# Kernel tuning notes

Measured on AMD Instinct MI355X. Metric: run time of the kernel, lower is better.

Reference implementation:

```python
import jax, jax.numpy as jnp
import numpy as np

B, T, D, H = 8, 2048, 1024, 128


def setup_inputs() -> dict:
    key = jax.random.key(0)
    k1, k2, k3, k4 = jax.random.split(key, 4)
    x = jax.random.normal(k1, (B, T, D), dtype=jnp.float32)
    # nn.Linear(D, H, bias=False): y = x @ W.T with W [H, D]; we store W as [D, H]
    Wq = jax.random.normal(k2, (D, H), dtype=jnp.float32) * (1.0 / np.sqrt(D))
    Wk = jax.random.normal(k3, (D, H), dtype=jnp.float32) * (1.0 / np.sqrt(D))
    Wv = jax.random.normal(k4, (D, H), dtype=jnp.float32) * (1.0 / np.sqrt(D))
    return {"x": x, "Wq": Wq, "Wk": Wk, "Wv": Wv}


def reference(x, Wq, Wk, Wv):
    # q, k, v projections (bias-free)
    q = jnp.einsum("btd,dh->bth", x, Wq)
    k = jnp.einsum("btd,dh->bth", x, Wk)
    v = jnp.einsum("btd,dh->bth", x, Wv)
    scale = 1.0 / jnp.sqrt(jnp.asarray(q.shape[-1], dtype=q.dtype))
    # full T x T score matrix, as in the original module
    scores = jnp.einsum("bqh,bkh->bqk", q, k) * scale
    T_ = x.shape[1]
    causal = jnp.tril(jnp.ones((T_, T_), dtype=bool))
    scores = jnp.where(causal[None, :, :], scores, -jnp.inf)
    weights = jax.nn.softmax(scores, axis=-1)
    # dropout is identity in eval mode (deterministic reference)
    return jnp.einsum("bqk,bkh->bqh", weights, v)
```

## Files before the change

kernel.cpp:

```cpp
#include <hip/hip_runtime.h>

typedef float  f32x4  __attribute__((ext_vector_type(4)));
typedef __bf16 bf16x8 __attribute__((ext_vector_type(8)));
typedef unsigned short u16;
typedef unsigned int   u32;
typedef u32 u32x4 __attribute__((ext_vector_type(4)));
typedef u16 u16x4 __attribute__((ext_vector_type(4)));
typedef u16 u16x8 __attribute__((ext_vector_type(8)));
typedef float f32x4v __attribute__((ext_vector_type(4)));

#define B_ 8
#define T_ 2048
#define D_ 1024
#define H_ 128
#define M_ (B_ * T_)

__device__ __forceinline__ u16 f2b(float f) {
  u32 u = __builtin_bit_cast(u32, f);
  u32 r = u + 0x7fffu + ((u >> 16) & 1u);
  return (u16)(r >> 16);
}

__global__ __launch_bounds__(256) void wt_kernel(const float* __restrict__ Wq,
                                                 const float* __restrict__ Wk,
                                                 const float* __restrict__ Wv,
                                                 u16* __restrict__ ws) {
  __shared__ u16 Ld[128 * 136];
  const float* W = (blockIdx.y == 0) ? Wq : (blockIdx.y == 1) ? Wk : Wv;
  u16* Wt = ws + (size_t)blockIdx.y * (D_ * H_);
  const int d0 = blockIdx.x * 128;
  const int t = threadIdx.x;
  for (int i = 0; i < 16; ++i) {
    int idx = i * 256 + t;
    int d = idx >> 5, h4 = (idx & 31) * 4;
    f32x4v wv = *(const f32x4v*)(W + (size_t)(d0 + d) * H_ + h4);
    u16x4 bv;
    bv[0] = f2b(wv[0]); bv[1] = f2b(wv[1]); bv[2] = f2b(wv[2]); bv[3] = f2b(wv[3]);
    *(u16x4*)(&Ld[d * 136 + h4]) = bv;
  }
  __syncthreads();
  for (int i = 0; i < 8; ++i) {
    int idx = i * 256 + t;
    int h = idx >> 4, d8 = (idx & 15) * 8;
    u16x8 ov;
    for (int j = 0; j < 8; ++j) ov[j] = Ld[(d8 + j) * 136 + h];
    *(u16x8*)(Wt + (size_t)h * D_ + d0 + d8) = ov;
  }
}

__global__ __launch_bounds__(256, 4) void qkv_gemm(const float* __restrict__ x,
                                                   const u16* __restrict__ Wt_all,
                                                   u16* __restrict__ Qb,
                                                   u16* __restrict__ Kb,
                                                   u16* __restrict__ Vt) {
  __shared__ __attribute__((aligned(16))) u16 As[32 * 40];
  __shared__ __attribute__((aligned(16))) u16 Bs[384 * 40];
  const int m0 = blockIdx.x * 32;
  const int t = threadIdx.x;
  const int lane = t & 63;
  const int w = t >> 6;
  const int wn = w * 96;
  const int li = lane & 15, q4 = lane >> 4;

  f32x4 acc[2][6];
  for (int i = 0; i < 2; ++i)
    for (int j = 0; j < 6; ++j) acc[i][j] = (f32x4){0.f, 0.f, 0.f, 0.f};

  f32x4v areg;
  u32x4 breg[6];
  const int arow = t >> 3, ac4 = (t & 7) * 4;

  auto load_tiles = [&](int kt) {
    const int k0 = kt * 32;
    areg = *(const f32x4v*)(x + (size_t)(m0 + arow) * D_ + k0 + ac4);
    for (int i2 = 0; i2 < 6; ++i2) {
      int idx = i2 * 256 + t;
      int row = idx >> 2, c8 = (idx & 3) * 8;
      breg[i2] = *(const u32x4*)(Wt_all + (size_t)row * D_ + k0 + c8);
    }
  };

  load_tiles(0);
  for (int kt = 0; kt < 32; ++kt) {
    __syncthreads();
    {
      u16x4 bv;
      bv[0] = f2b(areg[0]); bv[1] = f2b(areg[1]);
      bv[2] = f2b(areg[2]); bv[3] = f2b(areg[3]);
      *(u16x4*)(&As[arow * 40 + ac4]) = bv;
    }
    for (int i2 = 0; i2 < 6; ++i2) {
      int idx = i2 * 256 + t;
      int row = idx >> 2, c8 = (idx & 3) * 8;
      *(u32x4*)(&Bs[row * 40 + c8]) = breg[i2];
    }
    __syncthreads();
    if (kt + 1 < 32) load_tiles(kt + 1);

    bf16x8 af[2];
    for (int i = 0; i < 2; ++i)
      af[i] = *(const bf16x8*)(&As[(i * 16 + li) * 40 + q4 * 8]);
    for (int j = 0; j < 6; ++j) {
      bf16x8 bfr = *(const bf16x8*)(&Bs[(wn + j * 16 + li) * 40 + q4 * 8]);
      for (int i = 0; i < 2; ++i)
        acc[i][j] = __builtin_amdgcn_mfma_f32_16x16x32_bf16(af[i], bfr, acc[i][j], 0, 0, 0);
    }
  }

  const float qs = 0.12751740696864213f;
  const int bb = m0 >> 11;
  const int tl0 = (m0 & (T_ - 1)) + q4 * 4;
  for (int j = 0; j < 6; ++j) {
    int n = wn + j * 16 + li;
    int p = n >> 7, col = n & 127;
    if (p == 2) {
      for (int i = 0; i < 2; ++i) {
        u16x4 pv;
        for (int r = 0; r < 4; ++r) pv[r] = f2b(acc[i][j][r]);
        *(u16x4*)(Vt + (size_t)bb * (H_ * T_) + (size_t)col * T_ + tl0 + i * 16) = pv;
      }
    } else {
      u16* dst = (p == 0) ? Qb : Kb;
      float s = (p == 0) ? qs : 1.0f;
      for (int i = 0; i < 2; ++i)
        for (int r = 0; r < 4; ++r) {
          int mg = m0 + i * 16 + q4 * 4 + r;
          dst[(size_t)mg * H_ + col] = f2b(acc[i][j][r] * s);
        }
    }
  }
}

#define NSLOT_PER_B 36

__device__ __forceinline__ int slot_base(int qt) {
  return (qt < 8) ? 2 * (qt - 4) : (qt < 12) ? 8 + 3 * (qt - 8) : 20 + 4 * (qt - 12);
}

__global__ __launch_bounds__(512, 4) void flash_split(const u16* __restrict__ Qb,
                                                      const u16* __restrict__ Kb,
                                                      const u16* __restrict__ Vt,
                                                      float* __restrict__ Opart,
                                                      float* __restrict__ Ls,
                                                      float* __restrict__ out) {
  __shared__ __attribute__((aligned(16))) u16 Ks[64 * 136];
  __shared__ __attribute__((aligned(16))) u16 Vs[128 * 72];
  __shared__ __attribute__((aligned(16))) u16 Ps[128 * 72];

  int xb = blockIdx.x, qt = 15, split = 0;
  for (int q = 15; q >= 0; --q) {
    int ns = (2 * q + 9) >> 3;
    if (xb < ns) { qt = q; split = xb; break; }
    xb -= ns;
  }
  const int b = blockIdx.y;
  const int nkv = 2 * qt + 2;
  const int nsplit = (2 * qt + 9) >> 3;
  const int kv0t = split * 8;
  const int kv1t = (kv0t + 8 < nkv) ? kv0t + 8 : nkv;
  const int q0 = qt * 128;

  const int t = threadIdx.x;
  const int lane = t & 63;
  const int w = t >> 6;
  const int li = lane & 15, q4 = lane >> 4;

  bf16x8 qf[4];
  const int qrow = b * T_ + q0 + w * 16 + li;
  for (int kk = 0; kk < 4; ++kk)
    qf[kk] = *(const bf16x8*)(Qb + (size_t)qrow * H_ + kk * 32 + q4 * 8);

  f32x4 oacc[8];
  for (int i = 0; i < 8; ++i) oacc[i] = (f32x4){0.f, 0.f, 0.f, 0.f};
  float rs[4] = {0.f, 0.f, 0.f, 0.f};

  u32x4 kreg[2], vreg[2];
  auto load_tile = [&](int jt) {
    const int j0 = jt * 64;
    for (int rr = 0; rr < 2; ++rr) {
      int idx = rr * 512 + t;
      int row = idx >> 4, c = (idx & 15) * 8;
      kreg[rr] = *(const u32x4*)(Kb + (size_t)(b * T_ + j0 + row) * H_ + c);
    }
    for (int rr = 0; rr < 2; ++rr) {
      int idx = rr * 512 + t;
      int h = idx >> 3, c = (idx & 7) * 8;
      vreg[rr] = *(const u32x4*)(Vt + (size_t)b * (H_ * T_) + (size_t)h * T_ + j0 + c);
    }
  };

  load_tile(kv0t);
  for (int jt = kv0t; jt < kv1t; ++jt) {
    __syncthreads();
    for (int rr = 0; rr < 2; ++rr) {
      int idx = rr * 512 + t;
      int row = idx >> 4, c = (idx & 15) * 8;
      *(u32x4*)(&Ks[row * 136 + c]) = kreg[rr];
    }
    for (int rr = 0; rr < 2; ++rr) {
      int idx = rr * 512 + t;
      int h = idx >> 3, c = (idx & 7) * 8;
      *(u32x4*)(&Vs[h * 72 + c]) = vreg[rr];
    }
    __syncthreads();
    if (jt + 1 < kv1t) load_tile(jt + 1);

    f32x4 sacc[4];
    for (int jn = 0; jn < 4; ++jn) sacc[jn] = (f32x4){0.f, 0.f, 0.f, 0.f};
    for (int jn = 0; jn < 4; ++jn)
      for (int kk = 0; kk < 4; ++kk) {
        bf16x8 kf = *(const bf16x8*)(&Ks[(jn * 16 + li) * 136 + kk * 32 + q4 * 8]);
        sacc[jn] = __builtin_amdgcn_mfma_f32_16x16x32_bf16(qf[kk], kf, sacc[jn], 0, 0, 0);
      }

    if (jt >= 2 * qt) {
      const int j0 = jt * 64;
      for (int jn = 0; jn < 4; ++jn) {
        int jg = j0 + jn * 16 + li;
        for (int r = 0; r < 4; ++r) {
          int qg = q0 + w * 16 + q4 * 4 + r;
          if (jg > qg) sacc[jn][r] = -1e30f;
        }
      }
    }

    for (int jn = 0; jn < 4; ++jn)
      for (int r = 0; r < 4; ++r) {
        float p = exp2f(sacc[jn][r]);
        rs[r] += p;
        Ps[(w * 16 + q4 * 4 + r) * 72 + jn * 16 + li] = f2b(p);
      }

    for (int ks = 0; ks < 2; ++ks) {
      bf16x8 pa = *(const bf16x8*)(&Ps[(w * 16 + li) * 72 + ks * 32 + q4 * 8]);
      for (int hn = 0; hn < 8; ++hn) {
        bf16x8 vf = *(const bf16x8*)(&Vs[(hn * 16 + li) * 72 + ks * 32 + q4 * 8]);
        oacc[hn] = __builtin_amdgcn_mfma_f32_16x16x32_bf16(pa, vf, oacc[hn], 0, 0, 0);
      }
    }
  }

  float lr[4];
  for (int r = 0; r < 4; ++r) {
    float s = rs[r];
    for (int off = 1; off < 16; off <<= 1) s += __shfl_xor(s, off, 16);
    lr[r] = s;
  }

  if (nsplit == 1) {
    for (int hn = 0; hn < 8; ++hn)
      for (int r = 0; r < 4; ++r) {
        int qg = b * T_ + q0 + w * 16 + q4 * 4 + r;
        out[(size_t)qg * H_ + hn * 16 + li] = oacc[hn][r] / lr[r];
      }
  } else {
    const int slot = b * NSLOT_PER_B + slot_base(qt) + split;
    float* Od = Opart + (size_t)slot * (128 * 128);
    for (int hn = 0; hn < 8; ++hn)
      for (int r = 0; r < 4; ++r) {
        int qq = w * 16 + q4 * 4 + r;
        Od[qq * 128 + hn * 16 + li] = oacc[hn][r];
      }
    if (li == 0)
      for (int r = 0; r < 4; ++r)
        Ls[slot * 128 + w * 16 + q4 * 4 + r] = lr[r];
  }
}

__global__ __launch_bounds__(512) void flash_merge(const float* __restrict__ Opart,
                                                   const float* __restrict__ Ls,
                                                   float* __restrict__ out) {
  __shared__ float inv_l[128];
  const int qt = 4 + blockIdx.x;
  const int b = blockIdx.y;
  const int nsplit = (2 * qt + 9) >> 3;
  const int slot0 = b * NSLOT_PER_B + slot_base(qt);
  const int t = threadIdx.x;

  if (t < 128) {
    float L = 0.f;
    for (int s = 0; s < nsplit; ++s) L += Ls[(slot0 + s) * 128 + t];
    inv_l[t] = 1.0f / L;
  }
  __syncthreads();

  float* dst = out + ((size_t)b * T_ + (size_t)qt * 128) * H_;
  for (int i = 0; i < 8; ++i) {
    int e4 = i * 512 + t;
    int q = e4 >> 5;
    f32x4 acc = (f32x4){0.f, 0.f, 0.f, 0.f};
    for (int s = 0; s < nsplit; ++s) {
      f32x4 v = *(const f32x4*)(Opart + (size_t)(slot0 + s) * (128 * 128) + e4 * 4);
      acc[0] += v[0]; acc[1] += v[1]; acc[2] += v[2]; acc[3] += v[3];
    }
    float inv = inv_l[q];
    acc[0] *= inv; acc[1] *= inv; acc[2] *= inv; acc[3] *= inv;
    *(f32x4*)(dst + e4 * 4) = acc;
  }
}

extern "C" void kernel_launch(void* const* d_in, const int* in_sizes, int n_in,
                              void* d_out, int out_size, void* d_ws, size_t ws_size,
                              hipStream_t stream) {
  const float* x  = (const float*)d_in[0];
  const float* Wq = (const float*)d_in[1];
  const float* Wk = (const float*)d_in[2];
  const float* Wv = (const float*)d_in[3];
  float* out = (float*)d_out;

  u16* ws = (u16*)d_ws;
  u16* WtAll = ws;
  u16* Qb = ws + 3 * (size_t)(D_ * H_);
  u16* Kb = Qb + (size_t)M_ * H_;
  u16* Vt = Kb + (size_t)M_ * H_;
  float* Opart = (float*)(Vt + (size_t)M_ * H_);
  float* Ls = Opart + (size_t)8 * NSLOT_PER_B * 128 * 128;

  wt_kernel<<<dim3(8, 3), 256, 0, stream>>>(Wq, Wk, Wv, WtAll);
  qkv_gemm<<<dim3(512), 256, 0, stream>>>(x, WtAll, Qb, Kb, Vt);
  flash_split<<<dim3(40, 8), 512, 0, stream>>>(Qb, Kb, Vt, Opart, Ls, out);
  flash_merge<<<dim3(12, 8), 512, 0, stream>>>(Opart, Ls, out);
}
```

Baseline: 178.6 us.

## Retile QKV GEMM with double buffering and use swizzled direct-to-LDS loads in attention

```diff
diff --git a/kernel.cpp b/kernel.cpp
--- a/kernel.cpp
+++ b/kernel.cpp
@@ -19,6 +19,12 @@
   u32 u = __builtin_bit_cast(u32, f);
   u32 r = u + 0x7fffu + ((u >> 16) & 1u);
   return (u16)(r >> 16);
+}
+
+__device__ __forceinline__ void gl2lds16(const void* g, void* l) {
+  __builtin_amdgcn_global_load_lds(
+      (const __attribute__((address_space(1))) void*)g,
+      (__attribute__((address_space(3))) void*)l, 16, 0, 0);
 }
 
 __global__ __launch_bounds__(256) void wt_kernel(const float* __restrict__ Wq,
@@ -48,60 +54,63 @@
   }
 }
 
-__global__ __launch_bounds__(256, 4) void qkv_gemm(const float* __restrict__ x,
+__global__ __launch_bounds__(512, 4) void qkv_gemm(const float* __restrict__ x,
                                                    const u16* __restrict__ Wt_all,
                                                    u16* __restrict__ Qb,
                                                    u16* __restrict__ Kb,
                                                    u16* __restrict__ Vt) {
-  __shared__ __attribute__((aligned(16))) u16 As[32 * 40];
-  __shared__ __attribute__((aligned(16))) u16 Bs[384 * 40];
-  const int m0 = blockIdx.x * 32;
+  __shared__ __attribute__((aligned(16))) u16 As[2][64 * 40];
+  __shared__ __attribute__((aligned(16))) u16 Bs[2][192 * 40];
+  const int m0 = (int)(blockIdx.x >> 1) * 64;
+  const int n0 = (int)(blockIdx.x & 1) * 192;
   const int t = threadIdx.x;
   const int lane = t & 63;
   const int w = t >> 6;
-  const int wn = w * 96;
+  const int wm = (w & 1) * 32, wn = (w >> 1) * 48;
   const int li = lane & 15, q4 = lane >> 4;
 
-  f32x4 acc[2][6];
+  const int arow = t >> 3, ac4 = (t & 7) * 4;
+
+  f32x4 acc[2][3];
   for (int i = 0; i < 2; ++i)
-    for (int j = 0; j < 6; ++j) acc[i][j] = (f32x4){0.f, 0.f, 0.f, 0.f};
-
-  f32x4v areg;
-  u32x4 breg[6];
-  const int arow = t >> 3, ac4 = (t & 7) * 4;
-
-  auto load_tiles = [&](int kt) {
+    for (int j = 0; j < 3; ++j) acc[i][j] = (f32x4){0.f, 0.f, 0.f, 0.f};
+
+  f32x4v areg[2];
+  u16x4 breg[2][3];
+
+  auto load_tiles = [&](int kt, int s) {
     const int k0 = kt * 32;
-    areg = *(const f32x4v*)(x + (size_t)(m0 + arow) * D_ + k0 + ac4);
-    for (int i2 = 0; i2 < 6; ++i2) {
-      int idx = i2 * 256 + t;
-      int row = idx >> 2, c8 = (idx & 3) * 8;
-      breg[i2] = *(const u32x4*)(Wt_all + (size_t)row * D_ + k0 + c8);
+    areg[s] = *(const f32x4v*)(x + (size_t)(m0 + arow) * D_ + k0 + ac4);
+    for (int i2 = 0; i2 < 3; ++i2) {
+      int idx = i2 * 512 + t;
+      int row = idx >> 3, c4 = (idx & 7) * 4;
+      breg[s][i2] = *(const u16x4*)(Wt_all + (size_t)(n0 + row) * D_ + k0 + c4);
     }
   };
 
-  load_tiles(0);
+  load_tiles(0, 0);
+  load_tiles(1, 1);
   for (int kt = 0; kt < 32; ++kt) {
+    const int s = kt & 1;
+    {
+      u16x4 av;
+      av[0] = f2b(areg[s][0]); av[1] = f2b(areg[s][1]);
+      av[2] = f2b(areg[s][2]); av[3] = f2b(areg[s][3]);
+      *(u16x4*)(&As[s][arow * 40 + ac4]) = av;
+    }
+    for (int i2 = 0; i2 < 3; ++i2) {
+      int idx = i2 * 512 + t;
+      int row = idx >> 3, c4 = (idx & 7) * 4;
+      *(u16x4*)(&Bs[s][row * 40 + c4]) = breg[s][i2];
+    }
     __syncthreads();
-    {
-      u16x4 bv;
-      bv[0] = f2b(areg[0]); bv[1] = f2b(areg[1]);
-      bv[2] = f2b(areg[2]); bv[3] = f2b(areg[3]);
-      *(u16x4*)(&As[arow * 40 + ac4]) = bv;
-    }
-    for (int i2 = 0; i2 < 6; ++i2) {
-      int idx = i2 * 256 + t;
-      int row = idx >> 2, c8 = (idx & 3) * 8;
-      *(u32x4*)(&Bs[row * 40 + c8]) = breg[i2];
-    }
-    __syncthreads();
-    if (kt + 1 < 32) load_tiles(kt + 1);
+    if (kt + 2 < 32) load_tiles(kt + 2, s);
 
     bf16x8 af[2];
     for (int i = 0; i < 2; ++i)
-      af[i] = *(const bf16x8*)(&As[(i * 16 + li) * 40 + q4 * 8]);
-    for (int j = 0; j < 6; ++j) {
-      bf16x8 bfr = *(const bf16x8*)(&Bs[(wn + j * 16 + li) * 40 + q4 * 8]);
+      af[i] = *(const bf16x8*)(&As[s][(wm + i * 16 + li) * 40 + q4 * 8]);
+    for (int j = 0; j < 3; ++j) {
+      bf16x8 bfr = *(const bf16x8*)(&Bs[s][(wn + j * 16 + li) * 40 + q4 * 8]);
       for (int i = 0; i < 2; ++i)
         acc[i][j] = __builtin_amdgcn_mfma_f32_16x16x32_bf16(af[i], bfr, acc[i][j], 0, 0, 0);
     }
@@ -109,9 +118,9 @@
 
   const float qs = 0.12751740696864213f;
   const int bb = m0 >> 11;
-  const int tl0 = (m0 & (T_ - 1)) + q4 * 4;
-  for (int j = 0; j < 6; ++j) {
-    int n = wn + j * 16 + li;
+  const int tl0 = (m0 & (T_ - 1)) + wm + q4 * 4;
+  for (int j = 0; j < 3; ++j) {
+    int n = n0 + wn + j * 16 + li;
     int p = n >> 7, col = n & 127;
     if (p == 2) {
       for (int i = 0; i < 2; ++i) {
@@ -124,7 +133,7 @@
       float s = (p == 0) ? qs : 1.0f;
       for (int i = 0; i < 2; ++i)
         for (int r = 0; r < 4; ++r) {
-          int mg = m0 + i * 16 + q4 * 4 + r;
+          int mg = m0 + wm + i * 16 + q4 * 4 + r;
           dst[(size_t)mg * H_ + col] = f2b(acc[i][j][r] * s);
         }
     }
@@ -137,14 +146,14 @@
   return (qt < 8) ? 2 * (qt - 4) : (qt < 12) ? 8 + 3 * (qt - 8) : 20 + 4 * (qt - 12);
 }
 
-__global__ __launch_bounds__(512, 4) void flash_split(const u16* __restrict__ Qb,
+__global__ __launch_bounds__(512, 2) void flash_split(const u16* __restrict__ Qb,
                                                       const u16* __restrict__ Kb,
                                                       const u16* __restrict__ Vt,
                                                       float* __restrict__ Opart,
                                                       float* __restrict__ Ls,
                                                       float* __restrict__ out) {
-  __shared__ __attribute__((aligned(16))) u16 Ks[64 * 136];
-  __shared__ __attribute__((aligned(16))) u16 Vs[128 * 72];
+  __shared__ __attribute__((aligned(16))) u16 Ks[64 * 128];
+  __shared__ __attribute__((aligned(16))) u16 Vs[128 * 64];
   __shared__ __attribute__((aligned(16))) u16 Ps[128 * 72];
 
   int xb = blockIdx.x, qt = 15, split = 0;
@@ -174,47 +183,37 @@
   for (int i = 0; i < 8; ++i) oacc[i] = (f32x4){0.f, 0.f, 0.f, 0.f};
   float rs[4] = {0.f, 0.f, 0.f, 0.f};
 
-  u32x4 kreg[2], vreg[2];
-  auto load_tile = [&](int jt) {
+  for (int jt = kv0t; jt < kv1t; ++jt) {
     const int j0 = jt * 64;
-    for (int rr = 0; rr < 2; ++rr) {
-      int idx = rr * 512 + t;
-      int row = idx >> 4, c = (idx & 15) * 8;
-      kreg[rr] = *(const u32x4*)(Kb + (size_t)(b * T_ + j0 + row) * H_ + c);
-    }
-    for (int rr = 0; rr < 2; ++rr) {
-      int idx = rr * 512 + t;
-      int h = idx >> 3, c = (idx & 7) * 8;
-      vreg[rr] = *(const u32x4*)(Vt + (size_t)b * (H_ * T_) + (size_t)h * T_ + j0 + c);
-    }
-  };
-
-  load_tile(kv0t);
-  for (int jt = kv0t; jt < kv1t; ++jt) {
     __syncthreads();
-    for (int rr = 0; rr < 2; ++rr) {
-      int idx = rr * 512 + t;
-      int row = idx >> 4, c = (idx & 15) * 8;
-      *(u32x4*)(&Ks[row * 136 + c]) = kreg[rr];
-    }
-    for (int rr = 0; rr < 2; ++rr) {
-      int idx = rr * 512 + t;
-      int h = idx >> 3, c = (idx & 7) * 8;
-      *(u32x4*)(&Vs[h * 72 + c]) = vreg[rr];
+    for (int i = 0; i < 2; ++i) {
+      int seg = i * 8 + w;
+      {
+        int r = seg * 4 + (lane >> 4);
+        int c = (lane & 15) ^ (r & 7);
+        gl2lds16(Kb + (size_t)(b * T_ + j0 + r) * H_ + c * 8, &Ks[seg << 9]);
+      }
+      {
+        int r = seg * 8 + (lane >> 3);
+        int c = (lane & 7) ^ (r & 7);
+        gl2lds16(Vt + (size_t)b * (H_ * T_) + (size_t)r * T_ + j0 + c * 8,
+                 &Vs[seg << 9]);
+      }
     }
     __syncthreads();
-    if (jt + 1 < kv1t) load_tile(jt + 1);
 
     f32x4 sacc[4];
     for (int jn = 0; jn < 4; ++jn) sacc[jn] = (f32x4){0.f, 0.f, 0.f, 0.f};
-    for (int jn = 0; jn < 4; ++jn)
+    for (int jn = 0; jn < 4; ++jn) {
+      int row = jn * 16 + li;
       for (int kk = 0; kk < 4; ++kk) {
-        bf16x8 kf = *(const bf16x8*)(&Ks[(jn * 16 + li) * 136 + kk * 32 + q4 * 8]);
+        int phys = ((kk << 2) | q4) ^ (row & 7);
+        bf16x8 kf = *(const bf16x8*)(&Ks[row * 128 + phys * 8]);
         sacc[jn] = __builtin_amdgcn_mfma_f32_16x16x32_bf16(qf[kk], kf, sacc[jn], 0, 0, 0);
       }
+    }
 
     if (jt >= 2 * qt) {
-      const int j0 = jt * 64;
       for (int jn = 0; jn < 4; ++jn) {
         int jg = j0 + jn * 16 + li;
         for (int r = 0; r < 4; ++r) {
@@ -234,7 +233,9 @@
     for (int ks = 0; ks < 2; ++ks) {
       bf16x8 pa = *(const bf16x8*)(&Ps[(w * 16 + li) * 72 + ks * 32 + q4 * 8]);
       for (int hn = 0; hn < 8; ++hn) {
-        bf16x8 vf = *(const bf16x8*)(&Vs[(hn * 16 + li) * 72 + ks * 32 + q4 * 8]);
+        int row = hn * 16 + li;
+        int phys = ((ks << 2) | q4) ^ (row & 7);
+        bf16x8 vf = *(const bf16x8*)(&Vs[row * 64 + phys * 8]);
         oacc[hn] = __builtin_amdgcn_mfma_f32_16x16x32_bf16(pa, vf, oacc[hn], 0, 0, 0);
       }
     }
@@ -317,7 +318,7 @@
   float* Ls = Opart + (size_t)8 * NSLOT_PER_B * 128 * 128;
 
   wt_kernel<<<dim3(8, 3), 256, 0, stream>>>(Wq, Wk, Wv, WtAll);
-  qkv_gemm<<<dim3(512), 256, 0, stream>>>(x, WtAll, Qb, Kb, Vt);
+  qkv_gemm<<<dim3(512), 512, 0, stream>>>(x, WtAll, Qb, Kb, Vt);
   flash_split<<<dim3(40, 8), 512, 0, stream>>>(Qb, Kb, Vt, Opart, Ls, out);
   flash_merge<<<dim3(12, 8), 512, 0, stream>>>(Opart, Ls, out);
 }
```

New measurement: 173.8 us. 2.7% less time.
